# Kernel optimization log

Hardware: AMD Instinct MI355X
Metric: run time of the kernel (lower is better)

## Reference

```python
import jax, jax.numpy as jnp
import numpy as np

D_MODEL = 1024
N_HEADS = 16
D_K = D_MODEL // N_HEADS
B, T = 4, 2048


def setup_inputs() -> dict:
    key = jax.random.key(0)
    ks = jax.random.split(key, 6)
    scale = 1.0 / np.sqrt(D_MODEL)
    q = jax.random.normal(ks[0], (B, T, D_MODEL), dtype=jnp.float32)
    # causal mask: True = masked / ignored (upper triangle)
    causal = jnp.triu(jnp.ones((T, T), dtype=bool), k=1)
    mask = jnp.broadcast_to(causal, (B, 1, T, T))
    Wq = jax.random.normal(ks[1], (D_MODEL, D_MODEL), dtype=jnp.float32) * scale
    Wk = jax.random.normal(ks[2], (D_MODEL, D_MODEL), dtype=jnp.float32) * scale
    Wv = jax.random.normal(ks[3], (D_MODEL, D_MODEL), dtype=jnp.float32) * scale
    Wo = jax.random.normal(ks[4], (D_MODEL, D_MODEL), dtype=jnp.float32) * scale
    bq = jnp.zeros((D_MODEL,), jnp.float32)
    bk = jnp.zeros((D_MODEL,), jnp.float32)
    bv = jnp.zeros((D_MODEL,), jnp.float32)
    bo = jnp.zeros((D_MODEL,), jnp.float32)
    return {"q": q, "mask": mask, "Wq": Wq, "bq": bq, "Wk": Wk, "bk": bk,
            "Wv": Wv, "bv": bv, "Wo": Wo, "bo": bo}


def reference(q, mask, Wq, bq, Wk, bk, Wv, bv, Wo, bo):
    # Self-attention: k = v = q (module defaults). Weights stored torch-style
    # (out, in): y = x @ W.T + b.
    b, tq, _ = q.shape
    qh = (q @ Wq.T + bq).reshape(b, tq, N_HEADS, D_K).transpose(0, 2, 1, 3)  # (B,H,T,dk)
    kh = (q @ Wk.T + bk).reshape(b, tq, N_HEADS, D_K).transpose(0, 2, 1, 3)
    vh = (q @ Wv.T + bv).reshape(b, tq, N_HEADS, D_K).transpose(0, 2, 1, 3)
    attn = jnp.einsum('bhqd,bhkd->bhqk', qh, kh) / np.sqrt(D_K).astype(np.float32)
    attn = jnp.where(mask, -jnp.inf, attn)
    attn = jax.nn.softmax(attn, axis=-1)
    out = jnp.einsum('bhqk,bhkd->bhqd', attn, vh)
    out = out.transpose(0, 2, 1, 3).reshape(b, tq, D_MODEL)
    return out @ Wo.T + bo
```

## Files before the change

kernel.cpp:

```cpp
#include <hip/hip_runtime.h>
#include <hip/hip_bf16.h>
#include <stdint.h>

#define D_MODEL 1024
#define NH      16
#define DKH     64
#define BATCH   4
#define SEQ     2048
#define MROWS   (BATCH*SEQ)

typedef __hip_bfloat16 bf16;
typedef __attribute__((ext_vector_type(8))) short  bf16x8;
typedef __attribute__((ext_vector_type(4))) short  bf16x4;
typedef __attribute__((ext_vector_type(4))) float  f32x4;
typedef __attribute__((ext_vector_type(2))) unsigned int u32x2;

#define CEXP 0.18033688011112042f

__device__ __forceinline__ bf16 f2bf(float x){ return __float2bfloat16(x); }

__device__ __forceinline__ void gload_lds16(const void* g, void* l) {
  __builtin_amdgcn_global_load_lds(
      (const __attribute__((address_space(1))) unsigned int*)g,
      (__attribute__((address_space(3))) unsigned int*)l, 16, 0, 0);
}

__device__ __forceinline__ unsigned int pack2bf(float a, float b) {
  return __builtin_amdgcn_perm(__float_as_uint(b) + 0x8000u,
                               __float_as_uint(a) + 0x8000u, 0x07060302u);
}

__global__ __launch_bounds__(256)
void cvt_all(const float* __restrict__ q,
             const float* __restrict__ w0, const float* __restrict__ w1,
             const float* __restrict__ w2, const float* __restrict__ w3,
             bf16* __restrict__ qdst, bf16* __restrict__ wdst)
{
  const int NQB = (MROWS * D_MODEL) / 1024;
  const int bid = blockIdx.x;
  const float* src;
  bf16* dst;
  int i;
  if (bid < NQB) {
    src = q; dst = qdst;
    i = bid * 1024 + threadIdx.x * 4;
  } else {
    const int b2 = bid - NQB;
    const int w = b2 >> 10;
    src = (w == 0) ? w0 : (w == 1) ? w1 : (w == 2) ? w2 : w3;
    dst = wdst + (size_t)w * (D_MODEL * D_MODEL);
    i = (b2 & 1023) * 1024 + threadIdx.x * 4;
  }
  f32x4 v = *(const f32x4*)&src[i];
  union { bf16 e[4]; bf16x4 v4; } u;
  u.e[0] = f2bf(v[0]); u.e[1] = f2bf(v[1]);
  u.e[2] = f2bf(v[2]); u.e[3] = f2bf(v[3]);
  *(bf16x4*)&dst[i] = u.v4;
}

template <int MODE>
__global__ __launch_bounds__(512, 2)
void gemm8(const bf16* __restrict__ A, const bf16* __restrict__ W,
           const float* __restrict__ b0, const float* __restrict__ b1,
           const float* __restrict__ b2, void* __restrict__ Cbase)
{
  constexpr int K    = D_MODEL;
  constexpr int NT   = K / 64;
  constexpr int SLOT = (128 + 256) * 64;
  __shared__ __align__(16) short ring[3 * SLOT];

  const int tid  = threadIdx.x;
  const int lane = tid & 63;
  const int wave = tid >> 6;
  const int lm   = lane & 15;
  const int quad = lane >> 4;
  const int wm   = (wave >> 2) * 64;
  const int wn   = (wave & 3) * 64;
  const int bm   = blockIdx.x * 128;
  const int bn   = blockIdx.y * 256;

  const int rr    = tid >> 3;
  const int kperm = ((tid & 7) ^ (rr & 7)) * 8;
  const bf16* aS0 = A + (int64_t)(bm + rr) * K + kperm;
  const bf16* aS1 = aS0 + (int64_t)64 * K;
  const bf16* bS0 = W + (int64_t)(bn + rr) * K + kperm;
  const bf16* bS1 = bS0 + (int64_t)64 * K;
  const bf16* bS2 = bS0 + (int64_t)128 * K;
  const bf16* bS3 = bS0 + (int64_t)192 * K;

  f32x4 acc[4][4] = {};

#define STAGE8(T, S)                                                          \
  do {                                                                        \
    const int k0_ = (T) * 64;                                                 \
    short* As_ = &ring[(S) * SLOT];                                           \
    short* Bs_ = As_ + 128 * 64;                                              \
    gload_lds16(aS0 + k0_, &As_[tid * 8]);                                    \
    gload_lds16(aS1 + k0_, &As_[(tid + 512) * 8]);                            \
    gload_lds16(bS0 + k0_, &Bs_[tid * 8]);                                    \
    gload_lds16(bS1 + k0_, &Bs_[(tid + 512) * 8]);                            \
    gload_lds16(bS2 + k0_, &Bs_[(tid + 1024) * 8]);                           \
    gload_lds16(bS3 + k0_, &Bs_[(tid + 1536) * 8]);                           \
  } while (0)

  STAGE8(0, 0);
  STAGE8(1, 1);

#pragma unroll
  for (int t = 0; t < NT; ++t) {
    if (t < NT - 1) asm volatile("s_waitcnt vmcnt(6)" ::: "memory");
    else            asm volatile("s_waitcnt vmcnt(0)" ::: "memory");
    __builtin_amdgcn_s_barrier();
    asm volatile("" ::: "memory");
    if (t + 2 < NT) STAGE8(t + 2, (t + 2) % 3);

    const short* As = &ring[(t % 3) * SLOT];
    const short* Bs = As + 128 * 64;

    __builtin_amdgcn_s_setprio(1);
#pragma unroll
    for (int kk = 0; kk < 2; ++kk) {
      bf16x8 af[4], bfr[4];
#pragma unroll
      for (int i = 0; i < 4; ++i) {
        const int ra = wm + i * 16 + lm;
        af[i]  = *(const bf16x8*)&As[ra * 64 + (((kk * 4 + quad) ^ (ra & 7))) * 8];
        const int rb = wn + i * 16 + lm;
        bfr[i] = *(const bf16x8*)&Bs[rb * 64 + (((kk * 4 + quad) ^ (rb & 7))) * 8];
      }
#pragma unroll
      for (int i = 0; i < 4; ++i)
#pragma unroll
        for (int j = 0; j < 4; ++j)
          acc[i][j] = __builtin_amdgcn_mfma_f32_16x16x32_bf16(af[i], bfr[j], acc[i][j], 0, 0, 0);
    }
    __builtin_amdgcn_s_setprio(0);
  }
#undef STAGE8

  if constexpr (MODE == 1) {
    float* Cp = (float*)Cbase;
#pragma unroll
    for (int j = 0; j < 4; ++j) {
      const int n = bn + wn + j * 16 + lm;
      const float bv = b0[n];
#pragma unroll
      for (int i = 0; i < 4; ++i)
#pragma unroll
        for (int r = 0; r < 4; ++r) {
          const int m = bm + wm + i * 16 + quad * 4 + r;
          Cp[(int64_t)m * D_MODEL + n] = acc[i][j][r] + bv;
        }
    }
  } else {
    const int proj = bn >> 10;
    const int nl0  = bn & 1023;
    const float* bias = (proj == 0) ? b0 : (proj == 1) ? b1 : b2;
    if (proj == 2) {
      bf16* Vt = (bf16*)Cbase + 2 * (size_t)MROWS * D_MODEL;
#pragma unroll
      for (int j = 0; j < 4; ++j) {
        const int nl = nl0 + wn + j * 16 + lm;
        const float bv = bias[nl];
#pragma unroll
        for (int i = 0; i < 4; ++i) {
          const int m0 = bm + wm + i * 16 + quad * 4;
          const int64_t base = (int64_t)((m0 >> 11) * 16 + (nl >> 6)) * (DKH * SEQ)
                             + (nl & 63) * SEQ + (m0 & 2047);
          union { bf16 e[4]; bf16x4 v4; } u;
#pragma unroll
          for (int r = 0; r < 4; ++r) u.e[r] = f2bf(acc[i][j][r] + bv);
          *(bf16x4*)&Vt[base] = u.v4;
        }
      }
    } else {
      bf16* Cp = (bf16*)Cbase + (size_t)proj * MROWS * D_MODEL;
      const float sc = (proj == 0) ? CEXP : 1.0f;
#pragma unroll
      for (int j = 0; j < 4; ++j) {
        const int nl = nl0 + wn + j * 16 + lm;
        const float bv = bias[nl];
#pragma unroll
        for (int i = 0; i < 4; ++i)
#pragma unroll
          for (int r = 0; r < 4; ++r) {
            const int m = bm + wm + i * 16 + quad * 4 + r;
            Cp[(int64_t)m * D_MODEL + nl] = f2bf((acc[i][j][r] + bv) * sc);
          }
      }
    }
  }
}

__global__ __launch_bounds__(256)
void attn_causal(const bf16* __restrict__ Q, const bf16* __restrict__ Kg,
                 const bf16* __restrict__ Vt, bf16* __restrict__ O)
{
  __shared__ __align__(16) short lK[2][64 * 64];
  __shared__ __align__(16) short lV[2][64 * 64];
  __shared__ __align__(16) short lP[4 * 16 * 64];

  const int bid  = blockIdx.x;
  const int qt   = 31 - (bid >> 6);
  const int bh   = bid & 63;

  const int tid  = threadIdx.x;
  const int lane = tid & 63;
  const int wave = tid >> 6;
  const int lm   = lane & 15;
  const int quad = lane >> 4;
  const int qbase = qt * 64;
  const int64_t qkbase = (int64_t)((bh >> 4) * SEQ) * D_MODEL + (bh & 15) * DKH;
  const bf16* Kbase = Kg + qkbase;
  const bf16* Vbase = Vt + (int64_t)bh * DKH * SEQ;

  bf16x8 qf[2];
  {
    const bf16* qrow = Q + qkbase + (int64_t)(qbase + wave * 16 + lm) * D_MODEL;
    qf[0] = *(const bf16x8*)&qrow[quad * 8];
    qf[1] = *(const bf16x8*)&qrow[32 + quad * 8];
  }

  f32x4 o_acc[4] = {};
  float lsum = 0.f;

  const int srow = tid >> 3;
  const int sg   = (tid & 7) ^ (srow & 7);
  short* pw = &lP[wave * 1024];
  const int wqv = wave * 16 + lm;

  const bf16* kp0 = Kbase + (int64_t)srow        * D_MODEL + sg * 8;
  const bf16* kp1 = Kbase + (int64_t)(srow + 32) * D_MODEL + sg * 8;
  const bf16* vp0 = Vbase + (int64_t)srow        * SEQ + sg * 8;
  const bf16* vp1 = Vbase + (int64_t)(srow + 32) * SEQ + sg * 8;

#define STAGE(KB, BUF)                                                        \
  do {                                                                        \
    gload_lds16(kp0 + (int64_t)(KB) * D_MODEL, &lK[BUF][tid * 8]);            \
    gload_lds16(kp1 + (int64_t)(KB) * D_MODEL, &lK[BUF][(tid + 256) * 8]);    \
    gload_lds16(vp0 + (KB), &lV[BUF][tid * 8]);                               \
    gload_lds16(vp1 + (KB), &lV[BUF][(tid + 256) * 8]);                       \
  } while (0)

  STAGE(0, 0);

  for (int kt = 0; kt <= qt; ++kt) {
    const int cur = kt & 1;
    __syncthreads();
    if (kt < qt) STAGE((kt + 1) * 64, cur ^ 1);

    const short* lKc = lK[cur];
    const short* lVc = lV[cur];

    f32x4 s[4];
#pragma unroll
    for (int ni = 0; ni < 4; ++ni) {
      const int row = ni * 16 + lm;
      f32x4 zz = {};
      bf16x8 k0 = *(const bf16x8*)&lKc[row * 64 + ((quad       ^ (row & 7))) * 8];
      bf16x8 k1 = *(const bf16x8*)&lKc[row * 64 + (((4 + quad) ^ (row & 7))) * 8];
      zz = __builtin_amdgcn_mfma_f32_16x16x32_bf16(k0, qf[0], zz, 0, 0, 0);
      zz = __builtin_amdgcn_mfma_f32_16x16x32_bf16(k1, qf[1], zz, 0, 0, 0);
      s[ni] = zz;
    }

    if (kt == qt) {
#pragma unroll
      for (int ni = 0; ni < 4; ++ni) {
        const int kp = ni * 16 + quad * 4;
#pragma unroll
        for (int r = 0; r < 4; ++r)
          if (kp + r > wqv) s[ni][r] = -1e30f;
      }
    }

#pragma unroll
    for (int ni = 0; ni < 4; ++ni) {
      const float p0 = __builtin_amdgcn_exp2f(s[ni][0]);
      const float p1 = __builtin_amdgcn_exp2f(s[ni][1]);
      const float p2 = __builtin_amdgcn_exp2f(s[ni][2]);
      const float p3 = __builtin_amdgcn_exp2f(s[ni][3]);
      lsum += (p0 + p1) + (p2 + p3);
      u32x2 pk;
      pk[0] = pack2bf(p0, p1);
      pk[1] = pack2bf(p2, p3);
      *(u32x2*)&pw[lm * 64 + (((ni * 4 + quad) ^ lm)) * 4] = pk;
    }

#pragma unroll
    for (int kk = 0; kk < 2; ++kk) {
      const int h0 = (kk * 8 + 2 * quad) ^ lm;
      union { bf16x8 v; u32x2 h[2]; } pu;
      pu.h[0] = *(const u32x2*)&pw[lm * 64 + h0 * 4];
      pu.h[1] = *(const u32x2*)&pw[lm * 64 + (h0 ^ 1) * 4];
#pragma unroll
      for (int di = 0; di < 4; ++di) {
        const int vrow = di * 16 + lm;
        bf16x8 vb = *(const bf16x8*)&lVc[vrow * 64 + (((kk * 4 + quad) ^ (vrow & 7))) * 8];
        o_acc[di] = __builtin_amdgcn_mfma_f32_16x16x32_bf16(pu.v, vb, o_acc[di], 0, 0, 0);
      }
    }
  }
#undef STAGE

  lsum += __shfl_xor(lsum, 16);
  lsum += __shfl_xor(lsum, 32);
  const float linv = 1.0f / lsum;
  float lr[4];
#pragma unroll
  for (int r = 0; r < 4; ++r) lr[r] = __shfl(linv, quad * 4 + r);

#pragma unroll
  for (int di = 0; di < 4; ++di)
#pragma unroll
    for (int r = 0; r < 4; ++r) {
      const int qrow = qbase + wave * 16 + quad * 4 + r;
      O[qkbase + (int64_t)qrow * D_MODEL + di * 16 + lm] = f2bf(o_acc[di][r] * lr[r]);
    }
}

extern "C" void kernel_launch(void* const* d_in, const int* in_sizes, int n_in,
                              void* d_out, int out_size, void* d_ws, size_t ws_size,
                              hipStream_t stream)
{
  const float* q  = (const float*)d_in[0];
  const float* Wq = (const float*)d_in[2];
  const float* bq = (const float*)d_in[3];
  const float* Wk = (const float*)d_in[4];
  const float* bk = (const float*)d_in[5];
  const float* Wv = (const float*)d_in[6];
  const float* bv = (const float*)d_in[7];
  const float* Wo = (const float*)d_in[8];
  const float* bo = (const float*)d_in[9];
  float* out = (float*)d_out;

  const size_t NQ = (size_t)MROWS * D_MODEL;
  const size_t NW = (size_t)D_MODEL * D_MODEL;

  bf16* qb  = (bf16*)d_ws;
  bf16* Wb  = qb + NQ;
  bf16* Qw  = Wb + 4 * NW;
  bf16* Kw  = Qw + NQ;
  bf16* Vtw = Kw + NQ;

  cvt_all<<<dim3(NQ / 1024 + 4 * NW / 1024), 256, 0, stream>>>(
      q, Wq, Wk, Wv, Wo, qb, Wb);

  gemm8<0><<<dim3(MROWS / 128, 3 * D_MODEL / 256), 512, 0, stream>>>(
      qb, Wb, bq, bk, bv, Qw);

  attn_causal<<<dim3(BATCH * NH * (SEQ / 64)), 256, 0, stream>>>(Qw, Kw, Vtw, qb);

  gemm8<1><<<dim3(MROWS / 128, D_MODEL / 256), 512, 0, stream>>>(
      qb, Wb + 3 * NW, bo, bo, bo, out);
}
```

Baseline: 278.6 us.

## Keep P in registers via 16x16x16 MFMA and compute row sums with MFMA

Removes the LDS round-trip for the softmax probability tile. The S accumulator layout is fed directly as the A operand of 16x16x16 bf16 MFMAs for the PV product, and the row sums are computed with an MFMA against a ones vector instead of lane shuffles. It also switches to hardware v_cvt_pk_bf16_f32 packing and raises wave priority around the MFMA blocks. The trade is twice as many, smaller MFMAs plus extra MFMAs for the sum, and narrower 8-byte V reads from LDS.

```diff
diff --git a/kernel.cpp b/kernel.cpp
--- a/kernel.cpp
+++ b/kernel.cpp
@@ -25,10 +25,24 @@
       (__attribute__((address_space(3))) unsigned int*)l, 16, 0, 0);
 }
 
-__device__ __forceinline__ unsigned int pack2bf(float a, float b) {
-  return __builtin_amdgcn_perm(__float_as_uint(b) + 0x8000u,
-                               __float_as_uint(a) + 0x8000u, 0x07060302u);
-}
+__device__ __forceinline__ unsigned int cvtpk(float lo, float hi) {
+  unsigned int r;
+  asm("v_cvt_pk_bf16_f32 %0, %1, %2" : "=v"(r) : "v"(lo), "v"(hi));
+  return r;
+}
+
+#if __has_builtin(__builtin_amdgcn_mfma_f32_16x16x16bf16_1k)
+#define MFMA16(a, b, c) __builtin_amdgcn_mfma_f32_16x16x16bf16_1k(a, b, c, 0, 0, 0)
+#else
+__device__ __forceinline__ f32x4 mfma16_asm(bf16x4 a, bf16x4 b, f32x4 c) {
+  asm volatile("s_nop 2\n\t"
+               "v_mfma_f32_16x16x16_bf16 %0, %1, %2, %0\n\t"
+               "s_nop 7\n\ts_nop 2"
+               : "+v"(c) : "v"(a), "v"(b));
+  return c;
+}
+#define MFMA16(a, b, c) mfma16_asm(a, b, c)
+#endif
 
 __global__ __launch_bounds__(256)
 void cvt_all(const float* __restrict__ q,
@@ -198,7 +212,6 @@
 {
   __shared__ __align__(16) short lK[2][64 * 64];
   __shared__ __align__(16) short lV[2][64 * 64];
-  __shared__ __align__(16) short lP[4 * 16 * 64];
 
   const int bid  = blockIdx.x;
   const int qt   = 31 - (bid >> 6);
@@ -222,12 +235,12 @@
   }
 
   f32x4 o_acc[4] = {};
-  float lsum = 0.f;
+  f32x4 o_sum   = {};
+  const bf16x4 ones4 = {16256, 16256, 16256, 16256};
 
   const int srow = tid >> 3;
   const int sg   = (tid & 7) ^ (srow & 7);
-  short* pw = &lP[wave * 1024];
-  const int wqv = wave * 16 + lm;
+  const int wqv  = wave * 16 + lm;
 
   const bf16* kp0 = Kbase + (int64_t)srow        * D_MODEL + sg * 8;
   const bf16* kp1 = Kbase + (int64_t)(srow + 32) * D_MODEL + sg * 8;
@@ -253,6 +266,7 @@
     const short* lVc = lV[cur];
 
     f32x4 s[4];
+    __builtin_amdgcn_s_setprio(1);
 #pragma unroll
     for (int ni = 0; ni < 4; ++ni) {
       const int row = ni * 16 + lm;
@@ -263,6 +277,7 @@
       zz = __builtin_amdgcn_mfma_f32_16x16x32_bf16(k1, qf[1], zz, 0, 0, 0);
       s[ni] = zz;
     }
+    __builtin_amdgcn_s_setprio(0);
 
     if (kt == qt) {
 #pragma unroll
@@ -274,41 +289,38 @@
       }
     }
 
+    bf16x4 pk[4];
 #pragma unroll
     for (int ni = 0; ni < 4; ++ni) {
       const float p0 = __builtin_amdgcn_exp2f(s[ni][0]);
       const float p1 = __builtin_amdgcn_exp2f(s[ni][1]);
       const float p2 = __builtin_amdgcn_exp2f(s[ni][2]);
       const float p3 = __builtin_amdgcn_exp2f(s[ni][3]);
-      lsum += (p0 + p1) + (p2 + p3);
-      u32x2 pk;
-      pk[0] = pack2bf(p0, p1);
-      pk[1] = pack2bf(p2, p3);
-      *(u32x2*)&pw[lm * 64 + (((ni * 4 + quad) ^ lm)) * 4] = pk;
-    }
-
-#pragma unroll
-    for (int kk = 0; kk < 2; ++kk) {
-      const int h0 = (kk * 8 + 2 * quad) ^ lm;
-      union { bf16x8 v; u32x2 h[2]; } pu;
-      pu.h[0] = *(const u32x2*)&pw[lm * 64 + h0 * 4];
-      pu.h[1] = *(const u32x2*)&pw[lm * 64 + (h0 ^ 1) * 4];
+      union { unsigned int u[2]; bf16x4 v; } pu;
+      pu.u[0] = cvtpk(p0, p1);
+      pu.u[1] = cvtpk(p2, p3);
+      pk[ni] = pu.v;
+    }
+
+    __builtin_amdgcn_s_setprio(1);
+#pragma unroll
+    for (int ni = 0; ni < 4; ++ni) {
+      o_sum = MFMA16(pk[ni], ones4, o_sum);
 #pragma unroll
       for (int di = 0; di < 4; ++di) {
         const int vrow = di * 16 + lm;
-        bf16x8 vb = *(const bf16x8*)&lVc[vrow * 64 + (((kk * 4 + quad) ^ (vrow & 7))) * 8];
-        o_acc[di] = __builtin_amdgcn_mfma_f32_16x16x32_bf16(pu.v, vb, o_acc[di], 0, 0, 0);
-      }
-    }
+        const bf16x4 vb = *(const bf16x4*)&lVc[vrow * 64
+            + (((ni * 2 + (quad >> 1)) ^ (vrow & 7))) * 8 + (quad & 1) * 4];
+        o_acc[di] = MFMA16(pk[ni], vb, o_acc[di]);
+      }
+    }
+    __builtin_amdgcn_s_setprio(0);
   }
 #undef STAGE
 
-  lsum += __shfl_xor(lsum, 16);
-  lsum += __shfl_xor(lsum, 32);
-  const float linv = 1.0f / lsum;
   float lr[4];
 #pragma unroll
-  for (int r = 0; r < 4; ++r) lr[r] = __shfl(linv, quad * 4 + r);
+  for (int r = 0; r < 4; ++r) lr[r] = 1.0f / o_sum[r];
 
 #pragma unroll
   for (int di = 0; di < 4; ++di)
```

After: 277.9 us. About the same (-0.2%).
